# Optimization experiments

Measured on AMD Instinct MI355X. Metric: run time of the kernel, lower is better.

Reference implementation:

```python
import jax, jax.numpy as jnp
import numpy as np
from jax import lax

B = 64          # graphs per batch
N0 = 1024       # nodes per graph (equal-sized graphs -> static topk shapes)
DEG = 16        # avg degree
E = B * N0 * DEG
D_IN, D_H, D_OUT = 100, 128, 256
RATIO, EPS = 0.5, 1e-5


def _seg_sum(v, idx, n):
    return jax.ops.segment_sum(v, idx, num_segments=n)


def _gcn(x, src, dst, w_e, W, b, n):
    h = x @ W
    deg = 1.0 + _seg_sum(w_e, dst, n)          # +1 for self-loop
    dinv = lax.rsqrt(deg)
    norm = (dinv[src] * dinv[dst] * w_e)[:, None]
    return _seg_sum(h[src] * norm, dst, n) + h / deg[:, None] + b


def _graphnorm(x, w, bias, ms, nb, k):
    # PyG GraphNorm: per-graph mean/var with learnable mean_scale
    xg = x.reshape(nb, k, -1)
    mean = xg.mean(1, keepdims=True)
    sub = xg - ms * mean
    var = (sub * sub).mean(1, keepdims=True)
    return (w * sub * lax.rsqrt(var + EPS) + bias).reshape(nb * k, -1)


def _topk(x, src, dst, emask, p, nb, n_per):
    # TopKPooling (min_score=None): score = tanh(x.p/||p||), keep top ceil(r*n)
    k = int(np.ceil(RATIO * n_per))
    score = jnp.tanh((x @ p) / jnp.linalg.norm(p))
    vals, idx = lax.top_k(score.reshape(nb, n_per), k)            # [nb, k]
    perm = (idx + (jnp.arange(nb) * n_per)[:, None]).reshape(-1)
    x_new = x[perm] * vals.reshape(-1)[:, None]
    mapping = jnp.full((nb * n_per,), -1, jnp.int32).at[perm].set(
        jnp.arange(nb * k, dtype=jnp.int32))
    ns, nd = mapping[src], mapping[dst]
    valid = emask & (ns >= 0) & (nd >= 0)   # filter_adj as a persistent mask
    return x_new, jnp.where(valid, ns, 0), jnp.where(valid, nd, 0), valid, k


def _forward(x, edge_index, W1, b1, W2, b2, W3, b3,
             gn1_w, gn1_b, gn1_ms, gn2_w, gn2_b, gn2_ms,
             gn3_w, gn3_b, gn3_ms, p1, p2, p3):
    src, dst = edge_index[0], edge_index[1]
    emask = jnp.ones(src.shape, bool)
    Ws, bs = (W1, W2, W3), (b1, b2, b3)
    gw = (gn1_w, gn2_w, gn3_w)
    gb = (gn1_b, gn2_b, gn3_b)
    gm = (gn1_ms, gn2_ms, gn3_ms)
    ps = (p1, p2, p3)
    n_per = N0
    for i in range(3):
        n = B * n_per
        x = _gcn(x, src, dst, emask.astype(x.dtype), Ws[i], bs[i], n)
        x = _graphnorm(x, gw[i], gb[i], gm[i], B, n_per)
        x = jax.nn.relu(x)              # dropout: identity in eval mode
        x, src, dst, emask, n_per = _topk(x, src, dst, emask, ps[i], B, n_per)
    xg = x.reshape(B, n_per, D_OUT)
    # global mean/max pool then concat -> [B, 2*D_OUT]
    return jnp.concatenate([xg.mean(1), xg.max(1)], axis=1)


def setup_inputs():
    key = jax.random.key(0)
    ks = jax.random.split(key, 20)
    x = jax.random.normal(ks[0], (B * N0, D_IN), jnp.float32)
    # random edges within each graph, then offset by graph base index
    e = jax.random.randint(ks[1], (2, B, N0 * DEG), 0, N0, jnp.int32)
    edge_index = (e + (jnp.arange(B, dtype=jnp.int32) * N0)[None, :, None]).reshape(2, -1)
    batch = jnp.repeat(jnp.arange(B, dtype=jnp.int32), N0)
    inp = dict(x=x, edge_index=edge_index, batch=batch)
    dims = [(D_IN, D_H), (D_H, D_H), (D_H, D_OUT)]
    for i, (di, do) in enumerate(dims, 1):
        inp[f"W{i}"] = jax.random.normal(ks[1 + i], (di, do), jnp.float32) / np.sqrt(di)
        inp[f"b{i}"] = jnp.zeros((do,), jnp.float32)
        inp[f"gn{i}_w"] = jnp.ones((do,), jnp.float32)
        inp[f"gn{i}_b"] = jnp.zeros((do,), jnp.float32)
        inp[f"gn{i}_ms"] = jnp.ones((do,), jnp.float32)
        inp[f"p{i}"] = jax.random.normal(ks[10 + i], (do,), jnp.float32)
    return inp


def reference(x, edge_index, batch, W1, b1, W2, b2, W3, b3,
              gn1_w, gn1_b, gn1_ms, gn2_w, gn2_b, gn2_ms,
              gn3_w, gn3_b, gn3_ms, p1, p2, p3):
    del batch  # equal-sized graphs: grouping is encoded by constants B, N0
    return _forward(x, edge_index, W1, b1, W2, b2, W3, b3,
                    gn1_w, gn1_b, gn1_ms, gn2_w, gn2_b, gn2_ms,
                    gn3_w, gn3_b, gn3_ms, p1, p2, p3)
```

## Files before the change

kernel.cpp:

```cpp
#include <hip/hip_runtime.h>

#define GN_EPS 1e-5f

constexpr int NB   = 64;
constexpr int EPG  = 16384;
constexpr int ETOT = NB * EPG;
constexpr int NTOT = 64 * 1024;

__global__ void cmap_init_kernel(int* __restrict__ cmap) {
    int i = blockIdx.x * blockDim.x + threadIdx.x;
    if (i < NTOT) cmap[i] = i;
}

__global__ void compose_map_kernel(int* __restrict__ cmap, const int* __restrict__ mapping) {
    int i = blockIdx.x * blockDim.x + threadIdx.x;
    if (i >= NTOT) return;
    int c = cmap[i];
    cmap[i] = (c >= 0) ? mapping[c] : -1;
}

template <int NPG>
__global__ __launch_bounds__(1024) void csr_build_kernel(
        const int* __restrict__ ei, const int* __restrict__ cmap,
        int* __restrict__ cnt, int* __restrict__ offs, float* __restrict__ dinv,
        int* __restrict__ csr_src) {
    __shared__ int lcnt[NPG];
    __shared__ int lscan[NPG];
    const int g = blockIdx.x;
    const int t = threadIdx.x;
    const int ebase = g * EPG;
    constexpr int EPT = EPG / 1024;

    for (int i = t; i < NPG; i += 1024) lcnt[i] = 0;
    __syncthreads();

    int ms_[EPT], md_[EPT];
#pragma unroll
    for (int i = 0; i < EPT; i++) {
        int e = ebase + t + i * 1024;
        int s = cmap[ei[e]];
        int d = cmap[ei[ETOT + e]];
        bool ok = (s >= 0) && (d >= 0);
        ms_[i] = ok ? s : -1;
        md_[i] = ok ? (d - g * NPG) : 0;
        if (ok) atomicAdd(&lcnt[d - g * NPG], 1);
    }
    __syncthreads();

    if (t < NPG) lscan[t] = lcnt[t];
    __syncthreads();
    for (int d = 1; d < NPG; d <<= 1) {
        int x = 0;
        if (t < NPG && t >= d) x = lscan[t - d];
        __syncthreads();
        if (t < NPG) lscan[t] += x;
        __syncthreads();
    }
    if (t < NPG) {
        int v = lcnt[t];
        int excl = lscan[t] - v;
        cnt[g * NPG + t]  = v;
        offs[g * NPG + t] = ebase + excl;
        dinv[g * NPG + t] = rsqrtf(1.0f + (float)v);
        lcnt[t] = excl;
    }
    __syncthreads();

#pragma unroll
    for (int i = 0; i < EPT; i++) {
        if (ms_[i] >= 0) {
            int pos = atomicAdd(&lcnt[md_[i]], 1);
            csr_src[ebase + pos] = ms_[i];
        }
    }
}

__global__ __launch_bounds__(256) void gemm128_kernel(const float* __restrict__ A,
                                                      const float* __restrict__ W,
                                                      const float* __restrict__ dinv,
                                                      float* __restrict__ C,
                                                      int M, int N, int K) {
    __shared__ float As[16][132];
    __shared__ float Bs[16][132];
    const int bm = blockIdx.x * 128;
    const int bn = blockIdx.y * 128;
    const int tid = threadIdx.x;
    const int tx = tid & 15, ty = tid >> 4;

    const int arow = tid >> 1;
    const int ak   = (tid & 1) * 8;
    const int brow = tid >> 5;
    const int bc4  = (tid & 31) * 4;

    float acc[2][2][4][4] = {};

    for (int k0 = 0; k0 < K; k0 += 16) {
        {
            const float* ap = A + (size_t)(bm + arow) * K + k0 + ak;
            float4 a0 = {0,0,0,0}, a1 = {0,0,0,0};
            if (k0 + ak < K)     a0 = *reinterpret_cast<const float4*>(ap);
            if (k0 + ak + 4 < K) a1 = *reinterpret_cast<const float4*>(ap + 4);
            As[ak + 0][arow] = a0.x; As[ak + 1][arow] = a0.y;
            As[ak + 2][arow] = a0.z; As[ak + 3][arow] = a0.w;
            As[ak + 4][arow] = a1.x; As[ak + 5][arow] = a1.y;
            As[ak + 6][arow] = a1.z; As[ak + 7][arow] = a1.w;
        }
        {
            float4 b0 = {0,0,0,0}, b1 = {0,0,0,0};
            if (k0 + brow < K)
                b0 = *reinterpret_cast<const float4*>(W + (size_t)(k0 + brow) * N + bn + bc4);
            if (k0 + brow + 8 < K)
                b1 = *reinterpret_cast<const float4*>(W + (size_t)(k0 + brow + 8) * N + bn + bc4);
            *reinterpret_cast<float4*>(&Bs[brow][bc4])     = b0;
            *reinterpret_cast<float4*>(&Bs[brow + 8][bc4]) = b1;
        }
        __syncthreads();
#pragma unroll
        for (int k = 0; k < 16; k++) {
            float4 a0 = *reinterpret_cast<const float4*>(&As[k][ty * 4]);
            float4 a1 = *reinterpret_cast<const float4*>(&As[k][64 + ty * 4]);
            float4 b0 = *reinterpret_cast<const float4*>(&Bs[k][tx * 4]);
            float4 b1 = *reinterpret_cast<const float4*>(&Bs[k][64 + tx * 4]);
            const float av[2][4] = {{a0.x, a0.y, a0.z, a0.w}, {a1.x, a1.y, a1.z, a1.w}};
            const float bv[2][4] = {{b0.x, b0.y, b0.z, b0.w}, {b1.x, b1.y, b1.z, b1.w}};
#pragma unroll
            for (int qi = 0; qi < 2; qi++)
#pragma unroll
                for (int qj = 0; qj < 2; qj++)
#pragma unroll
                    for (int i = 0; i < 4; i++)
#pragma unroll
                        for (int j = 0; j < 4; j++)
                            acc[qi][qj][i][j] += av[qi][i] * bv[qj][j];
        }
        __syncthreads();
    }
#pragma unroll
    for (int qi = 0; qi < 2; qi++)
#pragma unroll
        for (int i = 0; i < 4; i++) {
            int row = bm + qi * 64 + ty * 4 + i;
            float dv = dinv[row];
#pragma unroll
            for (int qj = 0; qj < 2; qj++) {
                float4 o = {acc[qi][qj][i][0] * dv, acc[qi][qj][i][1] * dv,
                            acc[qi][qj][i][2] * dv, acc[qi][qj][i][3] * dv};
                *reinterpret_cast<float4*>(&C[(size_t)row * N + bn + qj * 64 + tx * 4]) = o;
            }
        }
}

template <int D4>
__global__ __launch_bounds__(256) void gather_kernel(
        const float* __restrict__ hs, const int* __restrict__ cnt,
        const int* __restrict__ offs, const float* __restrict__ dinv,
        const int* __restrict__ csr_src, const float* __restrict__ b,
        float* __restrict__ out, int n, int bpg) {
    constexpr int NPB = 256 / D4;
    int bid   = blockIdx.x;
    int xcd   = bid & 7;
    int slot  = bid >> 3;
    int graph = xcd + 8 * (slot / bpg);
    int local = slot % bpg;
    int vb    = graph * bpg + local;

    int v  = vb * NPB + threadIdx.x / D4;
    int f4 = threadIdx.x % D4;
    if (v >= n) return;
    const float4* h4 = reinterpret_cast<const float4*>(hs);
    int st = offs[v];
    int c  = cnt[v];
    float4 acc = h4[(size_t)v * D4 + f4];
    int j = 0;
    for (; j + 4 <= c; j += 4) {
        int s0 = csr_src[st + j],     s1 = csr_src[st + j + 1];
        int s2 = csr_src[st + j + 2], s3 = csr_src[st + j + 3];
        float4 h0 = h4[(size_t)s0 * D4 + f4];
        float4 h1 = h4[(size_t)s1 * D4 + f4];
        float4 h2 = h4[(size_t)s2 * D4 + f4];
        float4 h3 = h4[(size_t)s3 * D4 + f4];
        acc.x += h0.x + h1.x + h2.x + h3.x;
        acc.y += h0.y + h1.y + h2.y + h3.y;
        acc.z += h0.z + h1.z + h2.z + h3.z;
        acc.w += h0.w + h1.w + h2.w + h3.w;
    }
    for (; j < c; j++) {
        int s0 = csr_src[st + j];
        float4 h0 = h4[(size_t)s0 * D4 + f4];
        acc.x += h0.x; acc.y += h0.y; acc.z += h0.z; acc.w += h0.w;
    }
    float dv = dinv[v];
    float4 bb = reinterpret_cast<const float4*>(b)[f4];
    float4 o;
    o.x = acc.x * dv + bb.x;
    o.y = acc.y * dv + bb.y;
    o.z = acc.z * dv + bb.z;
    o.w = acc.w * dv + bb.w;
    reinterpret_cast<float4*>(out)[(size_t)v * D4 + f4] = o;
}

template <int D4>
__global__ __launch_bounds__(256) void gn_partial_kernel(
        const float* __restrict__ x, float* __restrict__ sum1, float* __restrict__ sum2,
        int n_per) {
    constexpr int GROUPS = 256 / D4;
    __shared__ float4 l1[256];
    __shared__ float4 l2[256];
    int g = blockIdx.x >> 3;
    int ch = blockIdx.x & 7;
    int f4 = threadIdx.x % D4;
    int grp = threadIdx.x / D4;
    int chunk = n_per / 8;
    int base = g * n_per + ch * chunk;
    const float4* x4 = reinterpret_cast<const float4*>(x);
    float4 s1 = {0.f, 0.f, 0.f, 0.f}, s2 = {0.f, 0.f, 0.f, 0.f};
    for (int i = grp; i < chunk; i += GROUPS) {
        float4 v = x4[(size_t)(base + i) * D4 + f4];
        s1.x += v.x; s1.y += v.y; s1.z += v.z; s1.w += v.w;
        s2.x += v.x * v.x; s2.y += v.y * v.y; s2.z += v.z * v.z; s2.w += v.w * v.w;
    }
    int t = threadIdx.x;
    l1[t] = s1; l2[t] = s2;
    __syncthreads();
    for (int str = 128; str >= D4; str >>= 1) {
        if (t < str) {
            float4 a = l1[t + str], b2 = l2[t + str];
            l1[t].x += a.x; l1[t].y += a.y; l1[t].z += a.z; l1[t].w += a.w;
            l2[t].x += b2.x; l2[t].y += b2.y; l2[t].z += b2.z; l2[t].w += b2.w;
        }
        __syncthreads();
    }
    if (t < D4) {
        size_t slot = (size_t)(g * 8 + ch) * (D4 * 4) + t * 4;
        *reinterpret_cast<float4*>(&sum1[slot]) = l1[t];
        *reinterpret_cast<float4*>(&sum2[slot]) = l2[t];
    }
}

__global__ void gn_final_kernel(const float* __restrict__ sum1, const float* __restrict__ sum2,
                                const float* __restrict__ ms, const float* __restrict__ w,
                                float* __restrict__ cmean, float* __restrict__ srw,
                                int n_per, int D, int total) {
    int t = blockIdx.x * blockDim.x + threadIdx.x;
    if (t >= total) return;
    int g = t / D;
    int f = t % D;
    float s1 = 0.f, s2 = 0.f;
    for (int ch = 0; ch < 8; ch++) {
        size_t slot = (size_t)(g * 8 + ch) * D + f;
        s1 += sum1[slot];
        s2 += sum2[slot];
    }
    float inv_n = 1.0f / (float)n_per;
    float mean = s1 * inv_n;
    float ex2  = s2 * inv_n;
    float m = ms[f];
    float var = ex2 - 2.f * m * mean * mean + m * m * mean * mean;
    cmean[t] = m * mean;
    srw[t]   = w[f] * rsqrtf(var + GN_EPS);
}

__global__ void pnorm3_kernel(const float* __restrict__ p0, const float* __restrict__ p1,
                              const float* __restrict__ p2, int d0, int d1, int d2,
                              float* __restrict__ out) {
    __shared__ float red[256];
    const float* p = (blockIdx.x == 0) ? p0 : (blockIdx.x == 1) ? p1 : p2;
    int d          = (blockIdx.x == 0) ? d0 : (blockIdx.x == 1) ? d1 : d2;
    int t = threadIdx.x;
    float v = (t < d) ? p[t] : 0.0f;
    red[t] = v * v;
    __syncthreads();
    for (int s = 128; s; s >>= 1) {
        if (t < s) red[t] += red[t + s];
        __syncthreads();
    }
    if (t == 0) out[blockIdx.x] = 1.0f / sqrtf(red[0]);
}

template <int DO>
__global__ __launch_bounds__(256) void gn_apply_score_kernel(
        float* __restrict__ x, const float* __restrict__ cmean, const float* __restrict__ srw,
        const float* __restrict__ bias, const float* __restrict__ p,
        const float* __restrict__ pinv, float* __restrict__ score, int n_per) {
    constexpr int V = DO / 64;
    int node = blockIdx.x * 4 + (threadIdx.x >> 6);
    int lane = threadIdx.x & 63;
    int g = node / n_per;
    float*       xr = x + (size_t)node * DO + lane * V;
    const float* cm = cmean + g * DO + lane * V;
    const float* sw = srw + g * DO + lane * V;
    const float* bb = bias + lane * V;
    const float* pp = p + lane * V;
    float dot = 0.f;
#pragma unroll
    for (int i = 0; i < V; i++) {
        float y = (xr[i] - cm[i]) * sw[i] + bb[i];
        y = fmaxf(y, 0.0f);
        xr[i] = y;
        dot += y * pp[i];
    }
#pragma unroll
    for (int off = 32; off; off >>= 1) dot += __shfl_xor(dot, off);
    if (lane == 0) score[node] = tanhf(dot * pinv[0]);
}

__global__ void topk_kernel(const float* __restrict__ score, int* __restrict__ mapping,
                            int* __restrict__ inv, int n_per, int k) {
    __shared__ float s[1024];
    int g = blockIdx.x;
    int i = threadIdx.x;
    float si = score[g * n_per + i];
    s[i] = si;
    __syncthreads();
    int rank = 0;
    for (int j = 0; j < n_per; j++) {
        float sj = s[j];
        rank += (sj > si) || (sj == si && j < i);
    }
    int old_g = g * n_per + i;
    if (rank < k) {
        int neu = g * k + rank;
        mapping[old_g] = neu;
        inv[neu] = old_g;
    } else {
        mapping[old_g] = -1;
    }
}

__global__ void permute_scale_kernel(const float* __restrict__ x, const int* __restrict__ inv,
                                     const float* __restrict__ score, float* __restrict__ xn,
                                     int total, int ldof4) {
    int t = blockIdx.x * blockDim.x + threadIdx.x;
    if (t >= total) return;
    int node = t >> ldof4;
    int f4   = t & ((1 << ldof4) - 1);
    int dof4 = 1 << ldof4;
    int old = inv[node];
    float sc = score[old];
    float4 v = reinterpret_cast<const float4*>(x)[(size_t)old * dof4 + f4];
    float4 o = {v.x * sc, v.y * sc, v.z * sc, v.w * sc};
    reinterpret_cast<float4*>(xn)[t] = o;
}

__global__ __launch_bounds__(1024) void pool_kernel(const float* __restrict__ x,
                                                    float* __restrict__ out, int n_per) {
    __shared__ float ssum[1024];
    __shared__ float smax[1024];
    int g = blockIdx.x;
    int f = threadIdx.x & 255;
    int ch = threadIdx.x >> 8;
    const float* xg = x + (size_t)g * n_per * 256;
    float s = 0.f, mx = -INFINITY;
    for (int i = ch; i < n_per; i += 4) {
        float v = xg[(size_t)i * 256 + f];
        s += v;
        mx = fmaxf(mx, v);
    }
    ssum[threadIdx.x] = s;
    smax[threadIdx.x] = mx;
    __syncthreads();
    if (ch == 0) {
#pragma unroll
        for (int c = 1; c < 4; c++) {
            s  += ssum[f + c * 256];
            mx  = fmaxf(mx, smax[f + c * 256]);
        }
        out[g * 512 + f]       = s / (float)n_per;
        out[g * 512 + 256 + f] = mx;
    }
}

static inline int cdiv_h(int a, int b) { return (a + b - 1) / b; }

extern "C" void kernel_launch(void* const* d_in, const int* in_sizes, int n_in,
                              void* d_out, int out_size, void* d_ws, size_t ws_size,
                              hipStream_t stream) {
    (void)in_sizes; (void)n_in; (void)out_size; (void)ws_size;

    const float* x_in = (const float*)d_in[0];
    const int*   ei   = (const int*)d_in[1];
    const float* Wm[3]  = {(const float*)d_in[3],  (const float*)d_in[9],  (const float*)d_in[15]};
    const float* bv[3]  = {(const float*)d_in[4],  (const float*)d_in[10], (const float*)d_in[16]};
    const float* gnw[3] = {(const float*)d_in[5],  (const float*)d_in[11], (const float*)d_in[17]};
    const float* gnb[3] = {(const float*)d_in[6],  (const float*)d_in[12], (const float*)d_in[18]};
    const float* gnm[3] = {(const float*)d_in[7],  (const float*)d_in[13], (const float*)d_in[19]};
    const float* pv[3]  = {(const float*)d_in[8],  (const float*)d_in[14], (const float*)d_in[20]};

    size_t off = 0;
    auto alloc = [&](size_t bytes) {
        void* p = (char*)d_ws + off;
        off += (bytes + 255) & ~(size_t)255;
        return p;
    };
    float* X1      = (float*)alloc((size_t)65536 * 128 * 4);
    float* H       = (float*)alloc((size_t)65536 * 128 * 4);
    float* X2      = (float*)alloc((size_t)32768 * 128 * 4);
    int*   csr_src = (int*)alloc((size_t)ETOT * 4);
    int*   cmap    = (int*)alloc(NTOT * 4);
    int*   cnt     = (int*)alloc(65536 * 4);
    int*   offs    = (int*)alloc(65536 * 4);
    float* dinv    = (float*)alloc(65536 * 4);
    float* score   = (float*)alloc(65536 * 4);
    int*   mapping = (int*)alloc(65536 * 4);
    int*   inv     = (int*)alloc(32768 * 4);
    float* sum1    = (float*)alloc(64 * 8 * 256 * 4);
    float* sum2    = (float*)alloc(64 * 8 * 256 * 4);
    float* cmean   = (float*)alloc(64 * 256 * 4);
    float* srw     = (float*)alloc(64 * 256 * 4);
    float* pinv    = (float*)alloc(256);

    const int nper[4] = {1024, 512, 256, 128};
    const int din[3]  = {100, 128, 128};
    const int dof[3]  = {128, 128, 256};

    cmap_init_kernel<<<NTOT / 256, 256, 0, stream>>>(cmap);
    pnorm3_kernel<<<3, 256, 0, stream>>>(pv[0], pv[1], pv[2], dof[0], dof[1], dof[2], pinv);

    for (int L = 0; L < 3; L++) {
        const int n    = NB * nper[L];
        const int k    = nper[L + 1];
        const int nn   = NB * k;
        const int D    = dof[L];
        const int dof4 = D / 4;
        const int ldof4 = (dof4 == 32) ? 5 : 6;
        const float* xin = (L == 0) ? x_in : X2;

        if (nper[L] == 1024)
            csr_build_kernel<1024><<<NB, 1024, 0, stream>>>(ei, cmap, cnt, offs, dinv, csr_src);
        else if (nper[L] == 512)
            csr_build_kernel<512><<<NB, 1024, 0, stream>>>(ei, cmap, cnt, offs, dinv, csr_src);
        else
            csr_build_kernel<256><<<NB, 1024, 0, stream>>>(ei, cmap, cnt, offs, dinv, csr_src);

        gemm128_kernel<<<dim3(n / 128, D / 128), 256, 0, stream>>>(xin, Wm[L], dinv, H,
                                                                   n, D, din[L]);

        if (dof4 == 32) {
            const int NPB = 8;
            const int bpg = nper[L] / NPB;
            gather_kernel<32><<<n / NPB, 256, 0, stream>>>(H, cnt, offs, dinv, csr_src,
                                                           bv[L], X1, n, bpg);
        } else {
            const int NPB = 4;
            const int bpg = nper[L] / NPB;
            gather_kernel<64><<<n / NPB, 256, 0, stream>>>(H, cnt, offs, dinv, csr_src,
                                                           bv[L], X1, n, bpg);
        }

        if (dof4 == 32)
            gn_partial_kernel<32><<<NB * 8, 256, 0, stream>>>(X1, sum1, sum2, nper[L]);
        else
            gn_partial_kernel<64><<<NB * 8, 256, 0, stream>>>(X1, sum1, sum2, nper[L]);
        gn_final_kernel<<<cdiv_h(NB * D, 256), 256, 0, stream>>>(sum1, sum2, gnm[L], gnw[L],
                                                                 cmean, srw, nper[L], D, NB * D);
        if (D == 128)
            gn_apply_score_kernel<128><<<n / 4, 256, 0, stream>>>(X1, cmean, srw, gnb[L],
                                                                  pv[L], pinv + L, score, nper[L]);
        else
            gn_apply_score_kernel<256><<<n / 4, 256, 0, stream>>>(X1, cmean, srw, gnb[L],
                                                                  pv[L], pinv + L, score, nper[L]);

        topk_kernel<<<NB, nper[L], 0, stream>>>(score, mapping, inv, nper[L], k);
        permute_scale_kernel<<<cdiv_h(nn * dof4, 256), 256, 0, stream>>>(X1, inv, score, X2,
                                                                         nn * dof4, ldof4);
        if (L < 2)
            compose_map_kernel<<<NTOT / 256, 256, 0, stream>>>(cmap, mapping);
    }

    pool_kernel<<<NB, 1024, 0, stream>>>(X2, (float*)d_out, nper[3]);
}
```

Before: 354.7 us.

## Replace quadratic rank-count top-k with radix-select and prefix-scan top-k

Swaps the O(N^2) per-thread rank counting in the top-k kernel for a 4-pass 8-bit radix select that finds the k-th key, followed by a block prefix scan that assigns output slots. This removes 1024 shared-memory reads per thread per graph. In exchange it adds many block-wide barriers and shared atomics. Output order becomes the index order within the greater-than and tied sets, not score-descending order, which may not match lax.top_k ordering.

```diff
diff --git a/kernel.cpp b/kernel.cpp
--- a/kernel.cpp
+++ b/kernel.cpp
@@ -304,24 +304,67 @@
     if (lane == 0) score[node] = tanhf(dot * pinv[0]);
 }
 
-__global__ void topk_kernel(const float* __restrict__ score, int* __restrict__ mapping,
-                            int* __restrict__ inv, int n_per, int k) {
-    __shared__ float s[1024];
-    int g = blockIdx.x;
-    int i = threadIdx.x;
-    float si = score[g * n_per + i];
-    s[i] = si;
-    __syncthreads();
-    int rank = 0;
-    for (int j = 0; j < n_per; j++) {
-        float sj = s[j];
-        rank += (sj > si) || (sj == si && j < i);
-    }
-    int old_g = g * n_per + i;
-    if (rank < k) {
-        int neu = g * k + rank;
-        mapping[old_g] = neu;
-        inv[neu] = old_g;
+template <int N, int K>
+__global__ __launch_bounds__(1024) void topk_radix_kernel(
+        const float* __restrict__ score, int* __restrict__ mapping,
+        int* __restrict__ inv) {
+    __shared__ int hist[256];
+    __shared__ int sscan[N];
+    __shared__ int sbyte, sneed;
+    const int g = blockIdx.x;
+    const int t = threadIdx.x;
+    float sc = score[g * N + t];
+    unsigned u = __float_as_uint(sc);
+    unsigned key = (u & 0x80000000u) ? ~u : (u | 0x80000000u);
+
+    unsigned prefix = 0;
+    int need = K;
+#pragma unroll
+    for (int shift = 24; shift >= 0; shift -= 8) {
+        if (t < 256) hist[t] = 0;
+        __syncthreads();
+        unsigned hm = (shift == 24) ? 0u : (0xFFFFFFFFu << (shift + 8));
+        if ((key & hm) == (prefix & hm))
+            atomicAdd(&hist[(key >> shift) & 255], 1);
+        __syncthreads();
+        if (t < 256) sscan[t] = hist[t];
+        __syncthreads();
+        for (int d = 1; d < 256; d <<= 1) {
+            int x = (t < 256 && t + d < 256) ? sscan[t + d] : 0;
+            __syncthreads();
+            if (t < 256) sscan[t] += x;
+            __syncthreads();
+        }
+        if (t < 256) {
+            int ge  = sscan[t];
+            int gt_ = (t + 1 < 256) ? sscan[t + 1] : 0;
+            if (ge >= need && gt_ < need) { sbyte = t; sneed = need - gt_; }
+        }
+        __syncthreads();
+        prefix |= ((unsigned)sbyte << shift);
+        need = sneed;
+        __syncthreads();
+    }
+    bool gt = key > prefix;
+    bool eq = (key == prefix);
+    sscan[t] = (gt ? (1 << 16) : 0) | (eq ? 1 : 0);
+    __syncthreads();
+    for (int d = 1; d < N; d <<= 1) {
+        int x = (t >= d) ? sscan[t - d] : 0;
+        __syncthreads();
+        sscan[t] += x;
+        __syncthreads();
+    }
+    int incl   = sscan[t];
+    int gtrank = (incl >> 16) - (gt ? 1 : 0);
+    int eqrank = (incl & 0xFFFF) - (eq ? 1 : 0);
+    int cntGT  = K - need;
+    bool sel = gt || (eq && (eqrank < need));
+    int old_g = g * N + t;
+    if (sel) {
+        int slot = gt ? gtrank : (cntGT + eqrank);
+        mapping[old_g] = g * K + slot;
+        inv[g * K + slot] = old_g;
     } else {
         mapping[old_g] = -1;
     }
@@ -460,7 +503,13 @@
             gn_apply_score_kernel<256><<<n / 4, 256, 0, stream>>>(X1, cmean, srw, gnb[L],
                                                                   pv[L], pinv + L, score, nper[L]);
 
-        topk_kernel<<<NB, nper[L], 0, stream>>>(score, mapping, inv, nper[L], k);
+        if (nper[L] == 1024)
+            topk_radix_kernel<1024, 512><<<NB, 1024, 0, stream>>>(score, mapping, inv);
+        else if (nper[L] == 512)
+            topk_radix_kernel<512, 256><<<NB, 512, 0, stream>>>(score, mapping, inv);
+        else
+            topk_radix_kernel<256, 128><<<NB, 256, 0, stream>>>(score, mapping, inv);
+
         permute_scale_kernel<<<cdiv_h(nn * dof4, 256), 256, 0, stream>>>(X1, inv, score, X2,
                                                                          nn * dof4, ldof4);
         if (L < 2)
```

Result: faster. 309.4 us (median of 2 runs) (-12.8%).
